# Performance work log

Measured on AMD Instinct MI355X. Metric: run time of the kernel, lower is better.

The kernel has to match this reference:

```python
import jax, jax.numpy as jnp
import numpy as np

TOKENS = 16384
IN_F = 2048
OUT_F = 2048
RANK = 32
GROUP = 64          # int4 scale group size
PAD = 256           # token padding multiple used by the fused activation quantizer
QMAX = 7.0          # signed int4 symmetric quantization


def setup_inputs() -> dict:
    key = jax.random.key(0)
    ks = jax.random.split(key, 7)
    x = jax.random.normal(ks[0], (TOKENS, IN_F), dtype=jnp.float32)
    # packed int4 weights: two signed nibbles per int8 lane
    qweight = jax.random.randint(ks[1], (OUT_F, IN_F // 2), -128, 128, dtype=jnp.int8)
    # per-group weight scales [in//group, out], strictly positive
    wscales = jnp.abs(jax.random.normal(ks[2], (IN_F // GROUP, OUT_F), dtype=jnp.float32)) * 0.01 + 1e-4
    # activation smoothing factors, positive and near 1
    smooth_factor = jnp.abs(jax.random.normal(ks[3], (IN_F,), dtype=jnp.float32)) * 0.5 + 0.75
    bias = jax.random.normal(ks[4], (OUT_F,), dtype=jnp.float32) * 0.01
    proj_down = jax.random.normal(ks[5], (IN_F, RANK), dtype=jnp.float32) * 0.02
    proj_up = jax.random.normal(ks[6], (OUT_F, RANK), dtype=jnp.float32) * 0.02
    return {"x": x, "qweight": qweight, "wscales": wscales,
            "smooth_factor": smooth_factor, "bias": bias,
            "proj_down": proj_down, "proj_up": proj_up}


def _unpack_int4(qweight):
    # low nibble = even input channel, high nibble = odd input channel; arithmetic shifts keep sign
    low = jnp.right_shift(jnp.left_shift(qweight, 4), 4)
    high = jnpp = jnp.right_shift(qweight, 4)
    w = jnp.stack([low, high], axis=-1).reshape(qweight.shape[0], qweight.shape[1] * 2)
    return w.astype(jnp.float32)  # [out, in], values in [-8, 7]


def _forward(x, qweight, wscales, smooth_factor, bias, proj_down, proj_up):
    T = x.shape[0]
    t_pad = ((T + PAD - 1) // PAD) * PAD
    # activation smoothing
    xs = x / smooth_factor
    xs_p = jnp.pad(xs, ((0, t_pad - T), (0, 0)))
    # per-token per-64-group symmetric int4 activation quantization
    xg = xs_p.reshape(t_pad, IN_F // GROUP, GROUP)
    amax = jnp.max(jnp.abs(xg), axis=-1)                       # [Tp, G]
    ascales = jnp.where(amax > 0, amax / QMAX, jnp.float32(1.0))
    qx = jnp.clip(jnp.round(xg / ascales[..., None]), -8.0, 7.0)
    xdq = (qx * ascales[..., None]).reshape(t_pad, IN_F)       # dequantized activations
    # dequantize packed int4 weights with per-group scales
    w = _unpack_int4(qweight)                                  # [out, in]
    wdq = (w.reshape(OUT_F, IN_F // GROUP, GROUP) * wscales.T[:, :, None]).reshape(OUT_F, IN_F)
    # packed GEMM (dequantized equivalent) + fused low-rank residual + bias
    y = xdq @ wdq.T                                            # [Tp, out]
    y = y + (xs_p @ proj_down) @ proj_up.T + bias
    return y[:T]


def reference(x, qweight, wscales, smooth_factor, bias, proj_down, proj_up):
    return _forward(x, qweight, wscales, smooth_factor, bias, proj_down, proj_up)
```

## Files before the change

### kernel.cpp

```cpp
#include <hip/hip_runtime.h>

#define TOKENS 16384
#define THALF 8192
#define INF 2048
#define OUTF 2048
#define RANK 32
#define BM 256
#define BN 256
#define NPER 32

typedef int   int32x4  __attribute__((ext_vector_type(4)));
typedef int   int32x2  __attribute__((ext_vector_type(2)));
typedef float floatx4  __attribute__((ext_vector_type(4)));
typedef short bf16x8   __attribute__((ext_vector_type(8)));
typedef _Float16 f16x8 __attribute__((ext_vector_type(8)));

typedef __attribute__((address_space(1))) const void gconst_t;
typedef __attribute__((address_space(3))) void ldsv_t;

__device__ __forceinline__ void gload_lds16(const void* g, void* l) {
  __builtin_amdgcn_global_load_lds((gconst_t*)g, (ldsv_t*)l, 16, 0, 0);
}

__device__ __forceinline__ unsigned short f2bf(float f) {
  unsigned u = __float_as_uint(f);
  unsigned r = (u + 0x7FFFu + ((u >> 16) & 1u)) >> 16;
  return (unsigned short)r;
}

__global__ __launch_bounds__(256) void unpack_kernel(const int* __restrict__ qw,
                                                     const float* __restrict__ wsc,
                                                     _Float16* __restrict__ wdq) {
  int idx = blockIdx.x * 256 + threadIdx.x;
  int o = idx >> 6;
  int ch = idx & 63;
  float ws = wsc[(size_t)(ch >> 1) * OUTF + o];
  const int4* src = (const int4*)qw + (size_t)idx * 4;
  _Float16* dst = wdq + (size_t)o * INF + ch * 32;
#pragma unroll
  for (int q = 0; q < 4; ++q) {
    int4 v = src[q];
    int e[4] = {v.x, v.y, v.z, v.w};
    alignas(16) _Float16 h[8];
#pragma unroll
    for (int j = 0; j < 4; ++j) {
      int lo = ((int)((unsigned)e[j] << 28)) >> 28;
      int hi = ((int)((unsigned)e[j] << 24)) >> 28;
      h[2 * j]     = (_Float16)((float)lo * ws);
      h[2 * j + 1] = (_Float16)((float)hi * ws);
    }
    *(int4*)(dst + q * 8) = *(const int4*)h;
  }
}

__global__ __launch_bounds__(256) void prep_pdT(const float* __restrict__ pd,
                                                unsigned short* __restrict__ pdT) {
  int idx = blockIdx.x * 256 + threadIdx.x;
  int r = idx >> 11, c = idx & 2047;
  pdT[idx] = f2bf(pd[(size_t)c * RANK + r]);
}

__global__ __launch_bounds__(256) void quant_kernel(
    const float* __restrict__ x, const float* __restrict__ smooth,
    const unsigned short* __restrict__ pdT,
    _Float16* __restrict__ xdq, float* __restrict__ tdown, int tbase) {
  __shared__ char lds[32768];
  int tid = threadIdx.x, lane = tid & 63, wid = tid >> 6;
  int t0rel = blockIdx.x * 32;
  int mi = wid >> 1, ni = wid & 1;
  floatx4 acc = {0.f, 0.f, 0.f, 0.f};

  floatx4 xv[8];
  floatx4 sm;
  int32x4 pv[4];

  auto issue_loads = [&](int kc) {
    const float* xb = x + (size_t)(tbase + t0rel + wid * 8) * INF + kc * 256 + lane * 4;
#pragma unroll
    for (int r = 0; r < 8; ++r) xv[r] = *(const floatx4*)(xb + r * INF);
    sm = *(const floatx4*)(smooth + kc * 256 + lane * 4);
#pragma unroll
    for (int q = 0; q < 4; ++q) {
      int flat = tid + q * 256;
      int row = flat >> 5, c16 = flat & 31;
      pv[q] = *(const int32x4*)((const char*)pdT + (size_t)row * 4096 + kc * 512 + c16 * 16);
    }
  };

  issue_loads(0);

  for (int kc = 0; kc < 8; ++kc) {
    floatx4 rsm;
    rsm[0] = 1.0f / sm[0]; rsm[1] = 1.0f / sm[1];
    rsm[2] = 1.0f / sm[2]; rsm[3] = 1.0f / sm[3];
#pragma unroll
    for (int q = 0; q < 4; ++q) {
      int flat = tid + q * 256;
      int row = flat >> 5, c16 = flat & 31;
      int byte = (row * 512 + c16 * 16) ^ ((row & 7) << 4);
      *(int32x4*)(lds + 16384 + byte) = pv[q];
    }
#pragma unroll
    for (int r = 0; r < 8; ++r) {
      floatx4 xs;
      xs[0] = xv[r][0] * rsm[0]; xs[1] = xv[r][1] * rsm[1];
      xs[2] = xv[r][2] * rsm[2]; xs[3] = xv[r][3] * rsm[3];
      float m4 = fmaxf(fmaxf(fabsf(xs[0]), fabsf(xs[1])),
                       fmaxf(fabsf(xs[2]), fabsf(xs[3])));
      m4 = fmaxf(m4, __shfl_xor(m4, 1, 64));
      m4 = fmaxf(m4, __shfl_xor(m4, 2, 64));
      m4 = fmaxf(m4, __shfl_xor(m4, 4, 64));
      m4 = fmaxf(m4, __shfl_xor(m4, 8, 64));
      float ascale = m4 > 0.f ? m4 / 7.0f : 1.0f;
      float rq = 1.0f / ascale;
      int tokrel = t0rel + wid * 8 + r;
      alignas(8) _Float16 hq[4];
#pragma unroll
      for (int b = 0; b < 4; ++b) {
        float qf = fminf(7.f, fmaxf(-8.f, rintf(xs[b] * rq)));
        hq[b] = (_Float16)(qf * ascale);
      }
      *(int32x2*)((char*)xdq + ((size_t)tokrel * INF + kc * 256 + lane * 4) * 2) =
          *(const int32x2*)hq;
      unsigned lo = (unsigned)f2bf(xs[0]) | ((unsigned)f2bf(xs[1]) << 16);
      unsigned hi = (unsigned)f2bf(xs[2]) | ((unsigned)f2bf(xs[3]) << 16);
      int lrow = wid * 8 + r;
      int xbyte = (lrow * 512 + lane * 8) ^ ((lrow & 7) << 4);
      int32x2 wv; wv[0] = (int)lo; wv[1] = (int)hi;
      *(int32x2*)(lds + xbyte) = wv;
    }
    __syncthreads();
    if (kc + 1 < 8) issue_loads(kc + 1);
#pragma unroll
    for (int ks = 0; ks < 8; ++ks) {
      int arow = mi * 16 + (lane & 15);
      int ab = (arow * 512 + ks * 64 + ((lane >> 4) << 4)) ^ ((arow & 7) << 4);
      bf16x8 av = *(const bf16x8*)(lds + ab);
      int brow = ni * 16 + (lane & 15);
      int bb = (brow * 512 + ks * 64 + ((lane >> 4) << 4)) ^ ((brow & 7) << 4);
      bf16x8 bv = *(const bf16x8*)(lds + 16384 + bb);
      acc = __builtin_amdgcn_mfma_f32_16x16x32_bf16(av, bv, acc, 0, 0, 0);
    }
    __syncthreads();
  }

  int trow = tbase + t0rel + mi * 16 + ((lane >> 4) << 2);
  int col = ni * 16 + (lane & 15);
#pragma unroll
  for (int r = 0; r < 4; ++r)
    tdown[(size_t)(trow + r) * RANK + col] = acc[r];
}

__global__ __launch_bounds__(512, 2) void gemm_kernel(
    const _Float16* __restrict__ xdq, const _Float16* __restrict__ wdq,
    const float* __restrict__ tdown, const float* __restrict__ pu,
    const float* __restrict__ bias, float* __restrict__ y,
    int tbase, int mPanels) {
  __shared__ char smem[131072];

  int tid = threadIdx.x;
  int lane = tid & 63;
  int wid = tid >> 6;
  int wm = wid >> 2, wn = wid & 3;

  int s = blockIdx.x;
  int xcd = s & 7, idx = s >> 3;
  int npan = ((xcd & 3) << 1) + (idx & 1);
  int mpan = (xcd >> 2) * (mPanels >> 1) + (idx >> 1);
  int o0 = npan * BN;
  int t0rel = mpan * BM;
  int t0abs = tbase + t0rel;

  floatx4 acc[8][4];
#pragma unroll
  for (int m = 0; m < 8; ++m)
#pragma unroll
    for (int n = 0; n < 4; ++n) acc[m][n] = (floatx4){0.f, 0.f, 0.f, 0.f};

  auto stageA = [&](int g, int h) {
    int dst = (g & 1) * 65536 + h * 16384;
#pragma unroll
    for (int i = 0; i < 2; ++i) {
      int f = i * 512 + tid;
      int row = f >> 3, sl = (f & 7) ^ (row & 7);
      gload_lds16((const char*)xdq + (size_t)(t0rel + h * 128 + row) * (INF * 2) + g * 128 + sl * 16,
                  smem + dst + i * 8192 + wid * 1024);
    }
  };
  auto stageB = [&](int g, int h) {
    int dst = (g & 1) * 65536 + 32768 + h * 16384;
#pragma unroll
    for (int i = 0; i < 2; ++i) {
      int f = i * 512 + tid;
      int row = f >> 3, sl = (f & 7) ^ (row & 7);
      gload_lds16((const char*)wdq + (size_t)(o0 + h * 128 + row) * (INF * 2) + g * 128 + sl * 16,
                  smem + dst + i * 8192 + wid * 1024);
    }
  };

  int l = lane & 15;
  int abase[2], bbase[2];
#pragma unroll
  for (int ks = 0; ks < 2; ++ks) {
    abase[ks] = wm * 16384 + l * 128 + ((((ks << 2) + (lane >> 4)) ^ (l & 7)) << 4);
    bbase[ks] = 32768 + (wn >> 1) * 16384 + ((wn & 1) * 64 + l) * 128 +
                ((((ks << 2) + (lane >> 4)) ^ (l & 7)) << 4);
  }

  stageB(0, 0); stageA(0, 0); stageB(0, 1); stageA(0, 1);
  stageB(1, 0); stageA(1, 0);

  f16x8 areg[4][2], breg0[2][2], breg1[2][2];

  for (int t = 0; t < NPER; ++t) {
    if (t == NPER - 1) asm volatile("s_waitcnt vmcnt(0)" ::: "memory");
    else               asm volatile("s_waitcnt vmcnt(4)" ::: "memory");
    __builtin_amdgcn_s_barrier();
    __builtin_amdgcn_sched_barrier(0);

    const char* sb = smem + (t & 1) * 65536;
    const char* pa0 = sb + abase[0];
    const char* pa1 = sb + abase[1];
    const char* pb0 = sb + bbase[0];
    const char* pb1 = sb + bbase[1];

#pragma unroll
    for (int j = 0; j < 4; ++j) {
      areg[j][0] = *(const f16x8*)(pa0 + j * 2048);
      areg[j][1] = *(const f16x8*)(pa1 + j * 2048);
    }
#pragma unroll
    for (int nf = 0; nf < 2; ++nf) {
      breg0[nf][0] = *(const f16x8*)(pb0 + nf * 2048);
      breg0[nf][1] = *(const f16x8*)(pb1 + nf * 2048);
    }
    if (t + 1 < NPER) stageB(t + 1, 1);
    asm volatile("s_waitcnt lgkmcnt(0)" ::: "memory");
    __builtin_amdgcn_sched_barrier(0);
    __builtin_amdgcn_s_setprio(1);
#pragma unroll
    for (int j = 0; j < 4; ++j)
#pragma unroll
      for (int nf = 0; nf < 2; ++nf) {
        acc[j][nf] = __builtin_amdgcn_mfma_f32_16x16x32_f16(areg[j][0], breg0[nf][0], acc[j][nf], 0, 0, 0);
        acc[j][nf] = __builtin_amdgcn_mfma_f32_16x16x32_f16(areg[j][1], breg0[nf][1], acc[j][nf], 0, 0, 0);
      }
    __builtin_amdgcn_s_setprio(0);
    __builtin_amdgcn_s_barrier();

#pragma unroll
    for (int nf = 0; nf < 2; ++nf) {
      breg1[nf][0] = *(const f16x8*)(pb0 + (2 + nf) * 2048);
      breg1[nf][1] = *(const f16x8*)(pb1 + (2 + nf) * 2048);
    }
    if (t + 1 < NPER) stageA(t + 1, 1);
    asm volatile("s_waitcnt lgkmcnt(0)" ::: "memory");
    __builtin_amdgcn_sched_barrier(0);
    __builtin_amdgcn_s_setprio(1);
#pragma unroll
    for (int j = 0; j < 4; ++j)
#pragma unroll
      for (int nf = 0; nf < 2; ++nf) {
        acc[j][2 + nf] = __builtin_amdgcn_mfma_f32_16x16x32_f16(areg[j][0], breg1[nf][0], acc[j][2 + nf], 0, 0, 0);
        acc[j][2 + nf] = __builtin_amdgcn_mfma_f32_16x16x32_f16(areg[j][1], breg1[nf][1], acc[j][2 + nf], 0, 0, 0);
      }
    __builtin_amdgcn_s_setprio(0);
    __builtin_amdgcn_s_barrier();

#pragma unroll
    for (int j = 0; j < 4; ++j) {
      areg[j][0] = *(const f16x8*)(pa0 + (4 + j) * 2048);
      areg[j][1] = *(const f16x8*)(pa1 + (4 + j) * 2048);
    }
    if (t + 2 < NPER) stageB(t + 2, 0);
    asm volatile("s_waitcnt lgkmcnt(0)" ::: "memory");
    __builtin_amdgcn_sched_barrier(0);
    __builtin_amdgcn_s_setprio(1);
#pragma unroll
    for (int j = 0; j < 4; ++j)
#pragma unroll
      for (int nf = 0; nf < 2; ++nf) {
        acc[4 + j][2 + nf] = __builtin_amdgcn_mfma_f32_16x16x32_f16(areg[j][0], breg1[nf][0], acc[4 + j][2 + nf], 0, 0, 0);
        acc[4 + j][2 + nf] = __builtin_amdgcn_mfma_f32_16x16x32_f16(areg[j][1], breg1[nf][1], acc[4 + j][2 + nf], 0, 0, 0);
      }
    __builtin_amdgcn_s_setprio(0);
    __builtin_amdgcn_s_barrier();

    if (t + 2 < NPER) stageA(t + 2, 0);
    __builtin_amdgcn_s_setprio(1);
#pragma unroll
    for (int j = 0; j < 4; ++j)
#pragma unroll
      for (int nf = 0; nf < 2; ++nf) {
        acc[4 + j][nf] = __builtin_amdgcn_mfma_f32_16x16x32_f16(areg[j][0], breg0[nf][0], acc[4 + j][nf], 0, 0, 0);
        acc[4 + j][nf] = __builtin_amdgcn_mfma_f32_16x16x32_f16(areg[j][1], breg0[nf][1], acc[4 + j][nf], 0, 0, 0);
      }
    __builtin_amdgcn_s_setprio(0);
    __builtin_amdgcn_s_barrier();
  }

  __syncthreads();

  unsigned short* td_lds = (unsigned short*)smem;
  unsigned short* pu_lds = (unsigned short*)(smem + 16384);
  {
    int row = tid >> 1, h = (tid & 1) * 16;
    const float* ts = tdown + (size_t)(t0abs + row) * RANK + h;
    const float* ps = pu + (size_t)(o0 + row) * RANK + h;
    unsigned tw[8], pw[8];
#pragma unroll
    for (int q = 0; q < 4; ++q) {
      float4 v = *(const float4*)(ts + q * 4);
      tw[q * 2 + 0] = (unsigned)f2bf(v.x) | ((unsigned)f2bf(v.y) << 16);
      tw[q * 2 + 1] = (unsigned)f2bf(v.z) | ((unsigned)f2bf(v.w) << 16);
      float4 p = *(const float4*)(ps + q * 4);
      pw[q * 2 + 0] = (unsigned)f2bf(p.x) | ((unsigned)f2bf(p.y) << 16);
      pw[q * 2 + 1] = (unsigned)f2bf(p.z) | ((unsigned)f2bf(p.w) << 16);
    }
    int4 s0, s1;
    s0.x = (int)tw[0]; s0.y = (int)tw[1]; s0.z = (int)tw[2]; s0.w = (int)tw[3];
    s1.x = (int)tw[4]; s1.y = (int)tw[5]; s1.z = (int)tw[6]; s1.w = (int)tw[7];
    *(int4*)(td_lds + row * 32 + h) = s0;
    *(int4*)(td_lds + row * 32 + h + 8) = s1;
    s0.x = (int)pw[0]; s0.y = (int)pw[1]; s0.z = (int)pw[2]; s0.w = (int)pw[3];
    s1.x = (int)pw[4]; s1.y = (int)pw[5]; s1.z = (int)pw[6]; s1.w = (int)pw[7];
    *(int4*)(pu_lds + row * 32 + h) = s0;
    *(int4*)(pu_lds + row * 32 + h + 8) = s1;
  }
  __syncthreads();

  bf16x8 ta[8], pb4[4];
  int koff8 = (lane >> 4) << 3;
#pragma unroll
  for (int m = 0; m < 8; ++m)
    ta[m] = *(const bf16x8*)&td_lds[((wm << 7) + (m << 4) + (lane & 15)) * 32 + koff8];
#pragma unroll
  for (int n = 0; n < 4; ++n)
    pb4[n] = *(const bf16x8*)&pu_lds[((wn << 6) + (n << 4) + (lane & 15)) * 32 + koff8];

#pragma unroll
  for (int n = 0; n < 4; ++n) {
    int oc = o0 + (wn << 6) + (n << 4) + (lane & 15);
    float bv = bias[oc];
#pragma unroll
    for (int m = 0; m < 8; ++m) {
      floatx4 c = acc[m][n];
      c = __builtin_amdgcn_mfma_f32_16x16x32_bf16(ta[m], pb4[n], c, 0, 0, 0);
#pragma unroll
      for (int r = 0; r < 4; ++r) {
        int tr = t0abs + (wm << 7) + (m << 4) + ((lane >> 4) << 2) + r;
        y[(size_t)tr * OUTF + oc] = c[r] + bv;
      }
    }
  }
}

extern "C" void kernel_launch(void* const* d_in, const int* in_sizes, int n_in,
                              void* d_out, int out_size, void* d_ws, size_t ws_size,
                              hipStream_t stream) {
  const float* x      = (const float*)d_in[0];
  const int*   qw     = (const int*)d_in[1];
  const float* wsc    = (const float*)d_in[2];
  const float* smooth = (const float*)d_in[3];
  const float* bias   = (const float*)d_in[4];
  const float* pd     = (const float*)d_in[5];
  const float* pu     = (const float*)d_in[6];
  float* y = (float*)d_out;

  char* ws = (char*)d_ws;
  unsigned short* pdT = (unsigned short*)((char*)d_out + (64u << 20));

  if (ws_size >= 77594624ULL) {
    _Float16* xdq = (_Float16*)ws;
    _Float16* wdq = (_Float16*)(ws + 67108864);
    float* tdown  = (float*)(ws + 67108864 + 8388608);
    unpack_kernel<<<512, 256, 0, stream>>>(qw, wsc, wdq);
    prep_pdT<<<256, 256, 0, stream>>>(pd, pdT);
    quant_kernel<<<TOKENS / 32, 256, 0, stream>>>(x, smooth, pdT, xdq, tdown, 0);
    gemm_kernel<<<8 * (TOKENS / BM), 512, 0, stream>>>(
        xdq, wdq, tdown, pu, bias, y, 0, TOKENS / BM);
  } else {
    _Float16* xdq = (_Float16*)ws;
    _Float16* wdq = (_Float16*)(ws + 33554432);
    float* tdown  = (float*)(ws + 33554432 + 8388608);
    unpack_kernel<<<512, 256, 0, stream>>>(qw, wsc, wdq);
    prep_pdT<<<256, 256, 0, stream>>>(pd, pdT);
    for (int c = 0; c < 2; ++c) {
      int tbase = c * THALF;
      quant_kernel<<<THALF / 32, 256, 0, stream>>>(x, smooth, pdT, xdq, tdown, tbase);
      gemm_kernel<<<8 * (THALF / BM), 512, 0, stream>>>(
          xdq, wdq, tdown, pu, bias, y, tbase, THALF / BM);
    }
  }
}
```

Before: 196.4 us.

## Restructure GEMM main loop into two phases with fewer barriers

```diff
diff --git a/kernel.cpp b/kernel.cpp
--- a/kernel.cpp
+++ b/kernel.cpp
@@ -210,7 +210,7 @@
   stageB(0, 0); stageA(0, 0); stageB(0, 1); stageA(0, 1);
   stageB(1, 0); stageA(1, 0);
 
-  f16x8 areg[4][2], breg0[2][2], breg1[2][2];
+  f16x8 a03[4][2], a47[4][2], breg[4][2];
 
   for (int t = 0; t < NPER; ++t) {
     if (t == NPER - 1) asm volatile("s_waitcnt vmcnt(0)" ::: "memory");
@@ -226,77 +226,44 @@
 
 #pragma unroll
     for (int j = 0; j < 4; ++j) {
-      areg[j][0] = *(const f16x8*)(pa0 + j * 2048);
-      areg[j][1] = *(const f16x8*)(pa1 + j * 2048);
-    }
-#pragma unroll
-    for (int nf = 0; nf < 2; ++nf) {
-      breg0[nf][0] = *(const f16x8*)(pb0 + nf * 2048);
-      breg0[nf][1] = *(const f16x8*)(pb1 + nf * 2048);
-    }
-    if (t + 1 < NPER) stageB(t + 1, 1);
-    asm volatile("s_waitcnt lgkmcnt(0)" ::: "memory");
+      a03[j][0] = *(const f16x8*)(pa0 + j * 2048);
+      a03[j][1] = *(const f16x8*)(pa1 + j * 2048);
+    }
+#pragma unroll
+    for (int nf = 0; nf < 4; ++nf) {
+      breg[nf][0] = *(const f16x8*)(pb0 + nf * 2048);
+      breg[nf][1] = *(const f16x8*)(pb1 + nf * 2048);
+    }
+    if (t + 1 < NPER) { stageB(t + 1, 1); stageA(t + 1, 1); }
+#pragma unroll
+    for (int j = 0; j < 4; ++j) {
+      a47[j][0] = *(const f16x8*)(pa0 + (4 + j) * 2048);
+      a47[j][1] = *(const f16x8*)(pa1 + (4 + j) * 2048);
+    }
+    asm volatile("s_waitcnt lgkmcnt(8)" ::: "memory");
     __builtin_amdgcn_sched_barrier(0);
     __builtin_amdgcn_s_setprio(1);
 #pragma unroll
     for (int j = 0; j < 4; ++j)
 #pragma unroll
-      for (int nf = 0; nf < 2; ++nf) {
-        acc[j][nf] = __builtin_amdgcn_mfma_f32_16x16x32_f16(areg[j][0], breg0[nf][0], acc[j][nf], 0, 0, 0);
-        acc[j][nf] = __builtin_amdgcn_mfma_f32_16x16x32_f16(areg[j][1], breg0[nf][1], acc[j][nf], 0, 0, 0);
+      for (int nf = 0; nf < 4; ++nf) {
+        acc[j][nf] = __builtin_amdgcn_mfma_f32_16x16x32_f16(a03[j][0], breg[nf][0], acc[j][nf], 0, 0, 0);
+        acc[j][nf] = __builtin_amdgcn_mfma_f32_16x16x32_f16(a03[j][1], breg[nf][1], acc[j][nf], 0, 0, 0);
       }
     __builtin_amdgcn_s_setprio(0);
+    asm volatile("s_waitcnt lgkmcnt(0)" ::: "memory");
     __builtin_amdgcn_s_barrier();
-
-#pragma unroll
-    for (int nf = 0; nf < 2; ++nf) {
-      breg1[nf][0] = *(const f16x8*)(pb0 + (2 + nf) * 2048);
-      breg1[nf][1] = *(const f16x8*)(pb1 + (2 + nf) * 2048);
-    }
-    if (t + 1 < NPER) stageA(t + 1, 1);
-    asm volatile("s_waitcnt lgkmcnt(0)" ::: "memory");
     __builtin_amdgcn_sched_barrier(0);
+    if (t + 2 < NPER) { stageB(t + 2, 0); stageA(t + 2, 0); }
     __builtin_amdgcn_s_setprio(1);
 #pragma unroll
     for (int j = 0; j < 4; ++j)
 #pragma unroll
-      for (int nf = 0; nf < 2; ++nf) {
-        acc[j][2 + nf] = __builtin_amdgcn_mfma_f32_16x16x32_f16(areg[j][0], breg1[nf][0], acc[j][2 + nf], 0, 0, 0);
-        acc[j][2 + nf] = __builtin_amdgcn_mfma_f32_16x16x32_f16(areg[j][1], breg1[nf][1], acc[j][2 + nf], 0, 0, 0);
+      for (int nf = 0; nf < 4; ++nf) {
+        acc[4 + j][nf] = __builtin_amdgcn_mfma_f32_16x16x32_f16(a47[j][0], breg[nf][0], acc[4 + j][nf], 0, 0, 0);
+        acc[4 + j][nf] = __builtin_amdgcn_mfma_f32_16x16x32_f16(a47[j][1], breg[nf][1], acc[4 + j][nf], 0, 0, 0);
       }
     __builtin_amdgcn_s_setprio(0);
-    __builtin_amdgcn_s_barrier();
-
-#pragma unroll
-    for (int j = 0; j < 4; ++j) {
-      areg[j][0] = *(const f16x8*)(pa0 + (4 + j) * 2048);
-      areg[j][1] = *(const f16x8*)(pa1 + (4 + j) * 2048);
-    }
-    if (t + 2 < NPER) stageB(t + 2, 0);
-    asm volatile("s_waitcnt lgkmcnt(0)" ::: "memory");
-    __builtin_amdgcn_sched_barrier(0);
-    __builtin_amdgcn_s_setprio(1);
-#pragma unroll
-    for (int j = 0; j < 4; ++j)
-#pragma unroll
-      for (int nf = 0; nf < 2; ++nf) {
-        acc[4 + j][2 + nf] = __builtin_amdgcn_mfma_f32_16x16x32_f16(areg[j][0], breg1[nf][0], acc[4 + j][2 + nf], 0, 0, 0);
-        acc[4 + j][2 + nf] = __builtin_amdgcn_mfma_f32_16x16x32_f16(areg[j][1], breg1[nf][1], acc[4 + j][2 + nf], 0, 0, 0);
-      }
-    __builtin_amdgcn_s_setprio(0);
-    __builtin_amdgcn_s_barrier();
-
-    if (t + 2 < NPER) stageA(t + 2, 0);
-    __builtin_amdgcn_s_setprio(1);
-#pragma unroll
-    for (int j = 0; j < 4; ++j)
-#pragma unroll
-      for (int nf = 0; nf < 2; ++nf) {
-        acc[4 + j][nf] = __builtin_amdgcn_mfma_f32_16x16x32_f16(areg[j][0], breg0[nf][0], acc[4 + j][nf], 0, 0, 0);
-        acc[4 + j][nf] = __builtin_amdgcn_mfma_f32_16x16x32_f16(areg[j][1], breg0[nf][1], acc[4 + j][nf], 0, 0, 0);
-      }
-    __builtin_amdgcn_s_setprio(0);
-    __builtin_amdgcn_s_barrier();
   }
 
   __syncthreads();
```

After: 198.9 us. No clear change (+1.3%).

## Restructure GEMM main loop into two-step unrolled ping-pong pipeline with finer-grained staging

Applied to the files above, without the earlier changes.

```diff
diff --git a/kernel.cpp b/kernel.cpp
--- a/kernel.cpp
+++ b/kernel.cpp
@@ -208,92 +208,183 @@
   }
 
   stageB(0, 0); stageA(0, 0); stageB(0, 1); stageA(0, 1);
-  stageB(1, 0); stageA(1, 0);
-
-  f16x8 areg[4][2], breg0[2][2], breg1[2][2];
-
-  for (int t = 0; t < NPER; ++t) {
-    if (t == NPER - 1) asm volatile("s_waitcnt vmcnt(0)" ::: "memory");
-    else               asm volatile("s_waitcnt vmcnt(4)" ::: "memory");
-    __builtin_amdgcn_s_barrier();
-    __builtin_amdgcn_sched_barrier(0);
-
-    const char* sb = smem + (t & 1) * 65536;
-    const char* pa0 = sb + abase[0];
-    const char* pa1 = sb + abase[1];
-    const char* pb0 = sb + bbase[0];
-    const char* pb1 = sb + bbase[1];
+  stageB(1, 0);
+  asm volatile("s_waitcnt vmcnt(2)" ::: "memory");
+  __builtin_amdgcn_s_barrier();
+
+  f16x8 a03[4][2], a47[4][2], b01[2][2], b23[2][2];
+
+  for (int i = 0; i < NPER / 2; ++i) {
+    int tA = 2 * i;
+    const char* p0 = smem;
+    const char* p1 = smem + 65536;
 
 #pragma unroll
     for (int j = 0; j < 4; ++j) {
-      areg[j][0] = *(const f16x8*)(pa0 + j * 2048);
-      areg[j][1] = *(const f16x8*)(pa1 + j * 2048);
+      a03[j][0] = *(const f16x8*)(p0 + abase[0] + j * 2048);
+      a03[j][1] = *(const f16x8*)(p0 + abase[1] + j * 2048);
     }
 #pragma unroll
     for (int nf = 0; nf < 2; ++nf) {
-      breg0[nf][0] = *(const f16x8*)(pb0 + nf * 2048);
-      breg0[nf][1] = *(const f16x8*)(pb1 + nf * 2048);
-    }
-    if (t + 1 < NPER) stageB(t + 1, 1);
-    asm volatile("s_waitcnt lgkmcnt(0)" ::: "memory");
-    __builtin_amdgcn_sched_barrier(0);
-    __builtin_amdgcn_s_setprio(1);
-#pragma unroll
-    for (int j = 0; j < 4; ++j)
-#pragma unroll
-      for (int nf = 0; nf < 2; ++nf) {
-        acc[j][nf] = __builtin_amdgcn_mfma_f32_16x16x32_f16(areg[j][0], breg0[nf][0], acc[j][nf], 0, 0, 0);
-        acc[j][nf] = __builtin_amdgcn_mfma_f32_16x16x32_f16(areg[j][1], breg0[nf][1], acc[j][nf], 0, 0, 0);
+      b01[nf][0] = *(const f16x8*)(p0 + bbase[0] + nf * 2048);
+      b01[nf][1] = *(const f16x8*)(p0 + bbase[1] + nf * 2048);
+    }
+    stageA(tA + 1, 0);
+    asm volatile("s_waitcnt lgkmcnt(8)" ::: "memory");
+    __builtin_amdgcn_s_barrier();
+    asm volatile("s_waitcnt lgkmcnt(0)" ::: "memory");
+    __builtin_amdgcn_sched_barrier(0);
+    __builtin_amdgcn_s_setprio(1);
+#pragma unroll
+    for (int j = 0; j < 4; ++j)
+#pragma unroll
+      for (int nf = 0; nf < 2; ++nf) {
+        acc[j][nf] = __builtin_amdgcn_mfma_f32_16x16x32_f16(a03[j][0], b01[nf][0], acc[j][nf], 0, 0, 0);
+        acc[j][nf] = __builtin_amdgcn_mfma_f32_16x16x32_f16(a03[j][1], b01[nf][1], acc[j][nf], 0, 0, 0);
       }
     __builtin_amdgcn_s_setprio(0);
     __builtin_amdgcn_s_barrier();
 
 #pragma unroll
     for (int nf = 0; nf < 2; ++nf) {
-      breg1[nf][0] = *(const f16x8*)(pb0 + (2 + nf) * 2048);
-      breg1[nf][1] = *(const f16x8*)(pb1 + (2 + nf) * 2048);
-    }
-    if (t + 1 < NPER) stageA(t + 1, 1);
-    asm volatile("s_waitcnt lgkmcnt(0)" ::: "memory");
-    __builtin_amdgcn_sched_barrier(0);
-    __builtin_amdgcn_s_setprio(1);
-#pragma unroll
-    for (int j = 0; j < 4; ++j)
-#pragma unroll
-      for (int nf = 0; nf < 2; ++nf) {
-        acc[j][2 + nf] = __builtin_amdgcn_mfma_f32_16x16x32_f16(areg[j][0], breg1[nf][0], acc[j][2 + nf], 0, 0, 0);
-        acc[j][2 + nf] = __builtin_amdgcn_mfma_f32_16x16x32_f16(areg[j][1], breg1[nf][1], acc[j][2 + nf], 0, 0, 0);
+      b23[nf][0] = *(const f16x8*)(p0 + bbase[0] + (2 + nf) * 2048);
+      b23[nf][1] = *(const f16x8*)(p0 + bbase[1] + (2 + nf) * 2048);
+    }
+    stageB(tA + 1, 1);
+    __builtin_amdgcn_s_barrier();
+    asm volatile("s_waitcnt lgkmcnt(0)" ::: "memory");
+    __builtin_amdgcn_sched_barrier(0);
+    __builtin_amdgcn_s_setprio(1);
+#pragma unroll
+    for (int j = 0; j < 4; ++j)
+#pragma unroll
+      for (int nf = 0; nf < 2; ++nf) {
+        acc[j][2 + nf] = __builtin_amdgcn_mfma_f32_16x16x32_f16(a03[j][0], b23[nf][0], acc[j][2 + nf], 0, 0, 0);
+        acc[j][2 + nf] = __builtin_amdgcn_mfma_f32_16x16x32_f16(a03[j][1], b23[nf][1], acc[j][2 + nf], 0, 0, 0);
       }
     __builtin_amdgcn_s_setprio(0);
     __builtin_amdgcn_s_barrier();
 
 #pragma unroll
     for (int j = 0; j < 4; ++j) {
-      areg[j][0] = *(const f16x8*)(pa0 + (4 + j) * 2048);
-      areg[j][1] = *(const f16x8*)(pa1 + (4 + j) * 2048);
-    }
-    if (t + 2 < NPER) stageB(t + 2, 0);
-    asm volatile("s_waitcnt lgkmcnt(0)" ::: "memory");
-    __builtin_amdgcn_sched_barrier(0);
-    __builtin_amdgcn_s_setprio(1);
-#pragma unroll
-    for (int j = 0; j < 4; ++j)
-#pragma unroll
-      for (int nf = 0; nf < 2; ++nf) {
-        acc[4 + j][2 + nf] = __builtin_amdgcn_mfma_f32_16x16x32_f16(areg[j][0], breg1[nf][0], acc[4 + j][2 + nf], 0, 0, 0);
-        acc[4 + j][2 + nf] = __builtin_amdgcn_mfma_f32_16x16x32_f16(areg[j][1], breg1[nf][1], acc[4 + j][2 + nf], 0, 0, 0);
-      }
-    __builtin_amdgcn_s_setprio(0);
-    __builtin_amdgcn_s_barrier();
-
-    if (t + 2 < NPER) stageA(t + 2, 0);
-    __builtin_amdgcn_s_setprio(1);
-#pragma unroll
-    for (int j = 0; j < 4; ++j)
-#pragma unroll
-      for (int nf = 0; nf < 2; ++nf) {
-        acc[4 + j][nf] = __builtin_amdgcn_mfma_f32_16x16x32_f16(areg[j][0], breg0[nf][0], acc[4 + j][nf], 0, 0, 0);
-        acc[4 + j][nf] = __builtin_amdgcn_mfma_f32_16x16x32_f16(areg[j][1], breg0[nf][1], acc[4 + j][nf], 0, 0, 0);
+      a47[j][0] = *(const f16x8*)(p0 + abase[0] + (4 + j) * 2048);
+      a47[j][1] = *(const f16x8*)(p0 + abase[1] + (4 + j) * 2048);
+    }
+    stageA(tA + 1, 1);
+    __builtin_amdgcn_s_barrier();
+    asm volatile("s_waitcnt lgkmcnt(0)" ::: "memory");
+    __builtin_amdgcn_sched_barrier(0);
+    __builtin_amdgcn_s_setprio(1);
+#pragma unroll
+    for (int j = 0; j < 4; ++j)
+#pragma unroll
+      for (int nf = 0; nf < 2; ++nf) {
+        acc[4 + j][2 + nf] = __builtin_amdgcn_mfma_f32_16x16x32_f16(a47[j][0], b23[nf][0], acc[4 + j][2 + nf], 0, 0, 0);
+        acc[4 + j][2 + nf] = __builtin_amdgcn_mfma_f32_16x16x32_f16(a47[j][1], b23[nf][1], acc[4 + j][2 + nf], 0, 0, 0);
+      }
+    __builtin_amdgcn_s_setprio(0);
+    __builtin_amdgcn_s_barrier();
+
+    if (tA + 2 < NPER) {
+      stageB(tA + 2, 0);
+      asm volatile("s_waitcnt vmcnt(2)" ::: "memory");
+    } else {
+      asm volatile("s_waitcnt vmcnt(0)" ::: "memory");
+    }
+    __builtin_amdgcn_s_barrier();
+    __builtin_amdgcn_sched_barrier(0);
+    __builtin_amdgcn_s_setprio(1);
+#pragma unroll
+    for (int j = 0; j < 4; ++j)
+#pragma unroll
+      for (int nf = 0; nf < 2; ++nf) {
+        acc[4 + j][nf] = __builtin_amdgcn_mfma_f32_16x16x32_f16(a47[j][0], b01[nf][0], acc[4 + j][nf], 0, 0, 0);
+        acc[4 + j][nf] = __builtin_amdgcn_mfma_f32_16x16x32_f16(a47[j][1], b01[nf][1], acc[4 + j][nf], 0, 0, 0);
+      }
+    __builtin_amdgcn_s_setprio(0);
+    __builtin_amdgcn_s_barrier();
+
+#pragma unroll
+    for (int j = 0; j < 4; ++j) {
+      a03[j][0] = *(const f16x8*)(p1 + abase[0] + j * 2048);
+      a03[j][1] = *(const f16x8*)(p1 + abase[1] + j * 2048);
+    }
+#pragma unroll
+    for (int nf = 0; nf < 2; ++nf) {
+      b01[nf][0] = *(const f16x8*)(p1 + bbase[0] + nf * 2048);
+      b01[nf][1] = *(const f16x8*)(p1 + bbase[1] + nf * 2048);
+    }
+    if (tA + 2 < NPER) stageA(tA + 2, 0);
+    asm volatile("s_waitcnt lgkmcnt(8)" ::: "memory");
+    __builtin_amdgcn_s_barrier();
+    asm volatile("s_waitcnt lgkmcnt(0)" ::: "memory");
+    __builtin_amdgcn_sched_barrier(0);
+    __builtin_amdgcn_s_setprio(1);
+#pragma unroll
+    for (int j = 0; j < 4; ++j)
+#pragma unroll
+      for (int nf = 0; nf < 2; ++nf) {
+        acc[j][nf] = __builtin_amdgcn_mfma_f32_16x16x32_f16(a03[j][0], b01[nf][0], acc[j][nf], 0, 0, 0);
+        acc[j][nf] = __builtin_amdgcn_mfma_f32_16x16x32_f16(a03[j][1], b01[nf][1], acc[j][nf], 0, 0, 0);
+      }
+    __builtin_amdgcn_s_setprio(0);
+    __builtin_amdgcn_s_barrier();
+
+#pragma unroll
+    for (int nf = 0; nf < 2; ++nf) {
+      b23[nf][0] = *(const f16x8*)(p1 + bbase[0] + (2 + nf) * 2048);
+      b23[nf][1] = *(const f16x8*)(p1 + bbase[1] + (2 + nf) * 2048);
+    }
+    if (tA + 2 < NPER) stageB(tA + 2, 1);
+    __builtin_amdgcn_s_barrier();
+    asm volatile("s_waitcnt lgkmcnt(0)" ::: "memory");
+    __builtin_amdgcn_sched_barrier(0);
+    __builtin_amdgcn_s_setprio(1);
+#pragma unroll
+    for (int j = 0; j < 4; ++j)
+#pragma unroll
+      for (int nf = 0; nf < 2; ++nf) {
+        acc[j][2 + nf] = __builtin_amdgcn_mfma_f32_16x16x32_f16(a03[j][0], b23[nf][0], acc[j][2 + nf], 0, 0, 0);
+        acc[j][2 + nf] = __builtin_amdgcn_mfma_f32_16x16x32_f16(a03[j][1], b23[nf][1], acc[j][2 + nf], 0, 0, 0);
+      }
+    __builtin_amdgcn_s_setprio(0);
+    __builtin_amdgcn_s_barrier();
+
+#pragma unroll
+    for (int j = 0; j < 4; ++j) {
+      a47[j][0] = *(const f16x8*)(p1 + abase[0] + (4 + j) * 2048);
+      a47[j][1] = *(const f16x8*)(p1 + abase[1] + (4 + j) * 2048);
+    }
+    if (tA + 2 < NPER) stageA(tA + 2, 1);
+    __builtin_amdgcn_s_barrier();
+    asm volatile("s_waitcnt lgkmcnt(0)" ::: "memory");
+    __builtin_amdgcn_sched_barrier(0);
+    __builtin_amdgcn_s_setprio(1);
+#pragma unroll
+    for (int j = 0; j < 4; ++j)
+#pragma unroll
+      for (int nf = 0; nf < 2; ++nf) {
+        acc[4 + j][2 + nf] = __builtin_amdgcn_mfma_f32_16x16x32_f16(a47[j][0], b23[nf][0], acc[4 + j][2 + nf], 0, 0, 0);
+        acc[4 + j][2 + nf] = __builtin_amdgcn_mfma_f32_16x16x32_f16(a47[j][1], b23[nf][1], acc[4 + j][2 + nf], 0, 0, 0);
+      }
+    __builtin_amdgcn_s_setprio(0);
+    __builtin_amdgcn_s_barrier();
+
+    if (tA + 3 < NPER) {
+      stageB(tA + 3, 0);
+      asm volatile("s_waitcnt vmcnt(2)" ::: "memory");
+    } else {
+      asm volatile("s_waitcnt vmcnt(0)" ::: "memory");
+    }
+    __builtin_amdgcn_s_barrier();
+    __builtin_amdgcn_sched_barrier(0);
+    __builtin_amdgcn_s_setprio(1);
+#pragma unroll
+    for (int j = 0; j < 4; ++j)
+#pragma unroll
+      for (int nf = 0; nf < 2; ++nf) {
+        acc[4 + j][nf] = __builtin_amdgcn_mfma_f32_16x16x32_f16(a47[j][0], b01[nf][0], acc[4 + j][nf], 0, 0, 0);
+        acc[4 + j][nf] = __builtin_amdgcn_mfma_f32_16x16x32_f16(a47[j][1], b01[nf][1], acc[4 + j][nf], 0, 0, 0);
       }
     __builtin_amdgcn_s_setprio(0);
     __builtin_amdgcn_s_barrier();
```

New measurement: 198.9 us. About the same (+1.3%).
